# Performance work log

Measured on AMD Instinct MI355X. Metric: run time of the kernel, lower is better.

Reference implementation:

```python
import jax, jax.numpy as jnp
import numpy as np

N_VERT, D = 100000, 128
N_EDGE, K, R = 20000, 8, 4


def setup_inputs() -> dict:
    key = jax.random.key(0)
    ks = jax.random.split(key, 16)
    s = 0.05
    return {
        'feats': jax.random.normal(ks[0], (N_VERT, D), dtype=jnp.float32),
        'edge_members': jax.random.randint(ks[1], (N_EDGE, K), 0, N_VERT),
        'adj_members': jax.random.randint(ks[2], (N_EDGE, R, K), 0, N_VERT),
        'ids': jnp.arange(N_EDGE),
        'epoch': 10,
        # VertexConv params (Linear(d,1) each)
        'wq': jax.random.normal(ks[3], (D, 1)) * s, 'bq': jnp.zeros((1,)),
        'wk': jax.random.normal(ks[4], (D, 1)) * s, 'bk': jnp.zeros((1,)),
        'wv': jax.random.normal(ks[5], (D, 1)) * s, 'bv': jnp.zeros((1,)),
        # EdgeConv MLP: Linear(d, d//4) -> ReLU -> Linear(d//4, 1)
        'W1': jax.random.normal(ks[6], (D, D // 4)) * s, 'b1': jnp.zeros((D // 4,)),
        'W2': jax.random.normal(ks[7], (D // 4, 1)) * s, 'b2': jnp.zeros((1,)),
        # final classifier Linear(d, 2)
        'Wfc': jax.random.normal(ks[8], (D, 2)) * s, 'bfc': jnp.zeros((2,)),
    }


def _vertex_conv(feats, members, wq, bq, wk, bk, wv, bv):
    # members: [E, K] vertex indices; aggregates each hyperedge's vertices into one feature.
    f = feats[members]                         # [E,K,d] irregular gather
    q = f @ wq + bq                            # [E,K,1]
    k = f @ wk + bk                            # [E,K,1]
    v = f @ wv + bv                            # [E,K,1]
    # score[e,j,l] = q[e,j]*k[e,l]; original softmaxes over the K-1 "other" vertices (l != j)
    S = q * jnp.swapaxes(k, -1, -2)            # [E,K,K]
    S = jnp.where(jnp.eye(members.shape[-1], dtype=bool), -jnp.inf, S)
    a = jax.nn.softmax(S, axis=-1)             # [E,K,K]
    di = jnp.tanh(jnp.einsum('ejl,elo->ejo', a, v))  # [E,K,1] per-vertex scalar gate
    return (di * f).sum(axis=1)                # [E,d]


def reference(feats, edge_members, adj_members, ids, epoch,
              wq, bq, wk, bk, wv, bv, W1, b1, W2, b2, Wfc, bfc):
    n = edge_members.shape[0]
    # epoch >= wu_e(=0): hyperedge feature from edge_dict
    xn = _vertex_conv(feats, edge_members, wq, bq, wk, bk, wv, bv)   # [N,d]
    # epoch >= wu_a(=5): hyperedge features from each vertex's adjacent edges
    xe = _vertex_conv(feats, adj_members.reshape(n * R, K),
                      wq, bq, wk, bk, wv, bv).reshape(n, R, -1)       # [N,R,d]
    ft = jnp.concatenate([xn[:, None, :], xe], axis=1)                # [N,1+R,d]
    # EdgeConv: attention over the 1+R candidate hyperedge feats
    sc = jax.nn.relu(ft @ W1 + b1) @ W2 + b2                          # [N,1+R,1]
    a = jax.nn.softmax(sc, axis=1)
    h = (a * ft).sum(axis=1)                                          # [N,d]
    # dropout in eval mode (identity), then sigmoid(Linear(d,2))
    return jax.nn.sigmoid(h @ Wfc + bfc)                              # [N,2]
```

## Files before the change

kernel.cpp:

```cpp
#include <hip/hip_runtime.h>
#include <math.h>

#define KK 8
#define DD 128
#define RR 4
#define NG 5
#define HID 32
#define NSLOT 48

typedef __attribute__((ext_vector_type(8))) short short8_t;
typedef __attribute__((ext_vector_type(4))) float f32x4_t;

__device__ __forceinline__ unsigned short f2bf(float x) {
    unsigned int u = __float_as_uint(x);
    unsigned int r = (u + 0x7FFFu + ((u >> 16) & 1u)) >> 16;
    return (unsigned short)r;
}
__device__ __forceinline__ float bf2f(unsigned short u) {
    return __uint_as_float((unsigned int)u << 16);
}

__global__ __launch_bounds__(256) void proj_mfma(
    const float* __restrict__ feats, int n_vert, int n_tg,
    const float* __restrict__ wq, const float* __restrict__ wk,
    const float* __restrict__ wv, const float* __restrict__ Wfc,
    const float* __restrict__ W1,
    const float* __restrict__ bq, const float* __restrict__ bk,
    const float* __restrict__ bv,
    unsigned short* __restrict__ proj)
{
    __shared__ short Bsh[12 * 64 * 8];

    const int t = threadIdx.x;
    const int wave = t >> 6, lane = t & 63;
    const int row = lane & 15;
    const int kg  = lane >> 4;

    #pragma unroll
    for (int q = 0; q < 3; ++q) {
        const int p = t + q * 256;
        const int ntks = p >> 6, plane = p & 63;
        const int nt = ntks >> 2, ks = ntks & 3;
        const int n  = nt * 16 + (plane & 15);
        const int k0 = ks * 32 + (plane >> 4) * 8;
        short8_t v;
        #pragma unroll
        for (int j = 0; j < 8; ++j) {
            const int k = k0 + j;
            float val;
            if      (n == 0) val = wq[k];
            else if (n == 1) val = wk[k];
            else if (n == 2) val = wv[k];
            else if (n == 3) val = Wfc[2 * k];
            else if (n == 4) val = Wfc[2 * k + 1];
            else if (n < 37) val = W1[k * HID + (n - 5)];
            else             val = 0.f;
            v[j] = (short)f2bf(val);
        }
        *(short8_t*)&Bsh[p * 8] = v;
    }

    const float bq0 = bq[0], bk0 = bk[0], bv0 = bv[0];
    __syncthreads();

    for (int tg = blockIdx.x; tg < n_tg; tg += gridDim.x) {
        const int mbase = (tg * 4 + wave) * 16;
        if (mbase >= n_vert) continue;

        long long arow = (long long)(mbase + row);
        if (arow >= n_vert) arow = n_vert - 1;
        const float* ar = &feats[arow * DD + kg * 8];
        float4 araw[8];
        #pragma unroll
        for (int ks = 0; ks < 4; ++ks) {
            araw[2 * ks]     = *(const float4*)&ar[ks * 32];
            araw[2 * ks + 1] = *(const float4*)&ar[ks * 32 + 4];
        }

        short8_t afrag[4];
        #pragma unroll
        for (int ks = 0; ks < 4; ++ks) {
            const float4 x0 = araw[2 * ks], x1 = araw[2 * ks + 1];
            short8_t a;
            a[0] = (short)f2bf(x0.x); a[1] = (short)f2bf(x0.y);
            a[2] = (short)f2bf(x0.z); a[3] = (short)f2bf(x0.w);
            a[4] = (short)f2bf(x1.x); a[5] = (short)f2bf(x1.y);
            a[6] = (short)f2bf(x1.z); a[7] = (short)f2bf(x1.w);
            afrag[ks] = a;
        }

        #pragma unroll
        for (int nt = 0; nt < 3; ++nt) {
            f32x4_t acc = {0.f, 0.f, 0.f, 0.f};
            #pragma unroll
            for (int ks = 0; ks < 4; ++ks) {
                const short8_t b = *(const short8_t*)&Bsh[((nt * 4 + ks) * 64 + lane) * 8];
                acc = __builtin_amdgcn_mfma_f32_16x16x32_bf16(afrag[ks], b, acc, 0, 0, 0);
            }
            const int col = nt * 16 + row;
            if (col < 37) {
                const int slot = (col < 5) ? col : (col + 3);
                float badd = 0.f;
                if      (col == 0) badd = bq0;
                else if (col == 1) badd = bk0;
                else if (col == 2) badd = bv0;
                #pragma unroll
                for (int r = 0; r < 4; ++r) {
                    const int vr = mbase + kg * 4 + r;
                    if (vr < n_vert)
                        proj[(long long)vr * NSLOT + slot] = f2bf(acc[r] + badd);
                }
            }
        }
    }
}

__global__ __launch_bounds__(256) void edge_fused(
    const int* __restrict__ edge_members,
    const int* __restrict__ adj_members,
    const unsigned short* __restrict__ proj,
    const float* __restrict__ b1, const float* __restrict__ W2,
    const float* __restrict__ b2, const float* __restrict__ bfc,
    float* __restrict__ out, int n_edge)
{
    __shared__ int   vidS[4][NG * KK];
    __shared__ float diS [4][NG * KK];
    __shared__ float ftfcS[4][NG][2];
    __shared__ float scS [4][NG];

    const int t = threadIdx.x;
    const int w = t >> 6;
    const int lane = t & 63;
    const int e = blockIdx.x * 4 + w;
    if (e >= n_edge) return;

    const int g = lane >> 3;
    const int j = lane & 7;
    const bool act = lane < NG * KK;

    int vid = 0;
    if (act) vid = (g == 0) ? edge_members[e * KK + j]
                            : adj_members[((e * RR) + (g - 1)) * KK + j];

    const uint4 qpu = *(const uint4*)&proj[(long long)vid * NSLOT];

    if (act) vidS[w][lane] = vid;
    asm volatile("s_waitcnt lgkmcnt(0)" ::: "memory");

    const int m = lane & 31;
    const int h = lane >> 5;
    float pv2[3][KK];
    #pragma unroll
    for (int p = 0; p < 3; ++p) {
        const int grp = (p << 1) | h;
        if (grp < NG) {
            #pragma unroll
            for (int r = 0; r < KK; ++r) {
                const int vr = vidS[w][grp * KK + r];
                pv2[p][r] = bf2f(proj[(long long)vr * NSLOT + 8 + m]);
            }
        }
    }

    const float qv  = bf2f((unsigned short)(qpu.x & 0xFFFFu));
    const float kv  = bf2f((unsigned short)(qpu.x >> 16));
    const float vv  = bf2f((unsigned short)(qpu.y & 0xFFFFu));
    const float pf0 = bf2f((unsigned short)(qpu.y >> 16));
    const float pf1 = bf2f((unsigned short)(qpu.z & 0xFFFFu));

    float k8[KK], v8[KK];
    #pragma unroll
    for (int r = 0; r < KK; ++r) {
        k8[r] = __shfl(kv, (g << 3) + r);
        v8[r] = __shfl(vv, (g << 3) + r);
    }
    float mx = -1e30f;
    float s[KK];
    #pragma unroll
    for (int r = 0; r < KK; ++r) {
        s[r] = qv * k8[r];
        if (r != j) mx = fmaxf(mx, s[r]);
    }
    float den = 0.f, num = 0.f;
    #pragma unroll
    for (int r = 0; r < KK; ++r) {
        if (r == j) continue;
        const float ex = expf(s[r] - mx);
        den += ex;
        num += ex * v8[r];
    }
    const float di = tanhf(num / den);

    float px = di * pf0, py = di * pf1;
    #pragma unroll
    for (int mm = 4; mm >= 1; mm >>= 1) {
        px += __shfl_xor(px, mm);
        py += __shfl_xor(py, mm);
    }
    if (act) {
        diS[w][lane] = di;
        if (j == 0) { ftfcS[w][g][0] = px; ftfcS[w][g][1] = py; }
    }
    asm volatile("s_waitcnt lgkmcnt(0)" ::: "memory");

    const float b1m = b1[m];
    const float w2m = W2[m];
    #pragma unroll
    for (int p = 0; p < 3; ++p) {
        const int grp = (p << 1) | h;
        if (grp < NG) {
            float acc = 0.f;
            #pragma unroll
            for (int r = 0; r < KK; ++r)
                acc += diS[w][grp * KK + r] * pv2[p][r];
            float hid = fmaxf(acc + b1m, 0.f) * w2m;
            #pragma unroll
            for (int mm = 16; mm >= 1; mm >>= 1) hid += __shfl_xor(hid, mm);
            if (m == 0) scS[w][grp] = hid + b2[0];
        }
    }
    asm volatile("s_waitcnt lgkmcnt(0)" ::: "memory");

    if (lane < 2) {
        float sc0[NG];
        float m5 = -1e30f;
        #pragma unroll
        for (int gg = 0; gg < NG; ++gg) { sc0[gg] = scS[w][gg]; m5 = fmaxf(m5, sc0[gg]); }
        float ssum = 0.f;
        #pragma unroll
        for (int gg = 0; gg < NG; ++gg) { sc0[gg] = expf(sc0[gg] - m5); ssum += sc0[gg]; }
        const float inv = 1.f / ssum;
        float hc = 0.f;
        #pragma unroll
        for (int gg = 0; gg < NG; ++gg) hc += sc0[gg] * inv * ftfcS[w][gg][lane];
        const float z = hc + bfc[lane];
        out[e * 2 + lane] = 1.f / (1.f + expf(-z));
    }
}

extern "C" void kernel_launch(void* const* d_in, const int* in_sizes, int n_in,
                              void* d_out, int out_size, void* d_ws, size_t ws_size,
                              hipStream_t stream) {
    const float* feats        = (const float*)d_in[0];
    const int*   edge_members = (const int*)  d_in[1];
    const int*   adj_members  = (const int*)  d_in[2];
    const float* wq  = (const float*)d_in[5];
    const float* bq  = (const float*)d_in[6];
    const float* wk  = (const float*)d_in[7];
    const float* bk  = (const float*)d_in[8];
    const float* wv  = (const float*)d_in[9];
    const float* bv  = (const float*)d_in[10];
    const float* W1  = (const float*)d_in[11];
    const float* b1  = (const float*)d_in[12];
    const float* W2  = (const float*)d_in[13];
    const float* b2  = (const float*)d_in[14];
    const float* Wfc = (const float*)d_in[15];
    const float* bfc = (const float*)d_in[16];
    float* out = (float*)d_out;

    const int n_vert = in_sizes[0] / DD;
    const int n_edge = in_sizes[1] / KK;

    unsigned short* proj = (unsigned short*)d_ws;

    const int n_mtiles = (n_vert + 15) / 16;
    const int n_tg = (n_mtiles + 3) / 4;
    const int grid = (n_tg < 640) ? n_tg : 640;

    proj_mfma<<<grid, 256, 0, stream>>>(
        feats, n_vert, n_tg, wq, wk, wv, Wfc, W1, bq, bk, bv, proj);

    edge_fused<<<(n_edge + 3) / 4, 256, 0, stream>>>(
        edge_members, adj_members, proj, b1, W2, b2, bfc, out, n_edge);
}
```

Measured before the change: 41.85 us.

## Fuse projection and edge kernels into one cooperative kernel with grid sync

Merges the per-vertex projection phase and the per-edge attention phase into a single cooperative launch separated by a grid-wide barrier. Blocks then loop persistently over edge groups instead of launching one block per four edges. The aim is to remove the second kernel launch and the gap between the two kernels. In exchange it adds host-side occupancy queries and a grid sync, and the edge phase is limited to at most 640 persistent blocks. A fallback to the original two-kernel path remains if the cooperative launch fails.

```diff
diff --git a/kernel.cpp b/kernel.cpp
--- a/kernel.cpp
+++ b/kernel.cpp
@@ -1,4 +1,5 @@
 #include <hip/hip_runtime.h>
+#include <hip/hip_cooperative_groups.h>
 #include <math.h>
 
 #define KK 8
@@ -20,19 +21,16 @@
     return __uint_as_float((unsigned int)u << 16);
 }
 
-__global__ __launch_bounds__(256) void proj_mfma(
+__device__ __forceinline__ void proj_phase(
     const float* __restrict__ feats, int n_vert, int n_tg,
     const float* __restrict__ wq, const float* __restrict__ wk,
     const float* __restrict__ wv, const float* __restrict__ Wfc,
     const float* __restrict__ W1,
     const float* __restrict__ bq, const float* __restrict__ bk,
     const float* __restrict__ bv,
-    unsigned short* __restrict__ proj)
-{
-    __shared__ short Bsh[12 * 64 * 8];
-
-    const int t = threadIdx.x;
-    const int wave = t >> 6, lane = t & 63;
+    unsigned short* __restrict__ proj,
+    short* Bsh, int t, int wave, int lane, int bid, int gsz)
+{
     const int row = lane & 15;
     const int kg  = lane >> 4;
 
@@ -63,7 +61,7 @@
     const float bq0 = bq[0], bk0 = bk[0], bv0 = bv[0];
     __syncthreads();
 
-    for (int tg = blockIdx.x; tg < n_tg; tg += gridDim.x) {
+    for (int tg = bid; tg < n_tg; tg += gsz) {
         const int mbase = (tg * 4 + wave) * 16;
         if (mbase >= n_vert) continue;
 
@@ -115,28 +113,20 @@
     }
 }
 
-__global__ __launch_bounds__(256) void edge_fused(
-    const int* __restrict__ edge_members,
-    const int* __restrict__ adj_members,
+__device__ __forceinline__ void edge_body(
+    const int* __restrict__ edge_members, const int* __restrict__ adj_members,
     const unsigned short* __restrict__ proj,
     const float* __restrict__ b1, const float* __restrict__ W2,
     const float* __restrict__ b2, const float* __restrict__ bfc,
-    float* __restrict__ out, int n_edge)
-{
-    __shared__ int   vidS[4][NG * KK];
-    __shared__ float diS [4][NG * KK];
-    __shared__ float ftfcS[4][NG][2];
-    __shared__ float scS [4][NG];
-
-    const int t = threadIdx.x;
-    const int w = t >> 6;
-    const int lane = t & 63;
-    const int e = blockIdx.x * 4 + w;
-    if (e >= n_edge) return;
-
+    float* __restrict__ out, int n_edge, int e,
+    int w, int lane, int (*vidS)[NG * KK], float (*diS)[NG * KK],
+    float (*ftfcS)[NG][2], float (*scS)[NG])
+{
     const int g = lane >> 3;
     const int j = lane & 7;
     const bool act = lane < NG * KK;
+    const int m = lane & 31;
+    const int h = lane >> 5;
 
     int vid = 0;
     if (act) vid = (g == 0) ? edge_members[e * KK + j]
@@ -147,8 +137,6 @@
     if (act) vidS[w][lane] = vid;
     asm volatile("s_waitcnt lgkmcnt(0)" ::: "memory");
 
-    const int m = lane & 31;
-    const int h = lane >> 5;
     float pv2[3][KK];
     #pragma unroll
     for (int p = 0; p < 3; ++p) {
@@ -236,6 +224,77 @@
         const float z = hc + bfc[lane];
         out[e * 2 + lane] = 1.f / (1.f + expf(-z));
     }
+}
+
+__global__ __launch_bounds__(256) void dhg_all(
+    const float* __restrict__ feats, int n_vert, int n_tg,
+    const int* __restrict__ edge_members, const int* __restrict__ adj_members,
+    int n_edge, int n_eg,
+    const float* __restrict__ wq, const float* __restrict__ wk,
+    const float* __restrict__ wv, const float* __restrict__ Wfc,
+    const float* __restrict__ W1,
+    const float* __restrict__ bq, const float* __restrict__ bk,
+    const float* __restrict__ bv,
+    const float* __restrict__ b1, const float* __restrict__ W2,
+    const float* __restrict__ b2, const float* __restrict__ bfc,
+    unsigned short* __restrict__ proj, float* __restrict__ out)
+{
+    __shared__ short Bsh[12 * 64 * 8];
+    __shared__ int   vidS[4][NG * KK];
+    __shared__ float diS [4][NG * KK];
+    __shared__ float ftfcS[4][NG][2];
+    __shared__ float scS [4][NG];
+
+    const int t = threadIdx.x;
+    const int wave = t >> 6, lane = t & 63;
+
+    proj_phase(feats, n_vert, n_tg, wq, wk, wv, Wfc, W1, bq, bk, bv, proj,
+               Bsh, t, wave, lane, blockIdx.x, gridDim.x);
+
+    cooperative_groups::this_grid().sync();
+
+    for (int eg = blockIdx.x; eg < n_eg; eg += gridDim.x) {
+        const int e = eg * 4 + wave;
+        if (e >= n_edge) continue;
+        edge_body(edge_members, adj_members, proj, b1, W2, b2, bfc, out, n_edge,
+                  e, wave, lane, vidS, diS, ftfcS, scS);
+    }
+}
+
+__global__ __launch_bounds__(256) void proj_mfma(
+    const float* __restrict__ feats, int n_vert, int n_tg,
+    const float* __restrict__ wq, const float* __restrict__ wk,
+    const float* __restrict__ wv, const float* __restrict__ Wfc,
+    const float* __restrict__ W1,
+    const float* __restrict__ bq, const float* __restrict__ bk,
+    const float* __restrict__ bv,
+    unsigned short* __restrict__ proj)
+{
+    __shared__ short Bsh[12 * 64 * 8];
+    const int t = threadIdx.x;
+    proj_phase(feats, n_vert, n_tg, wq, wk, wv, Wfc, W1, bq, bk, bv, proj,
+               Bsh, t, t >> 6, t & 63, blockIdx.x, gridDim.x);
+}
+
+__global__ __launch_bounds__(256) void edge_fused(
+    const int* __restrict__ edge_members,
+    const int* __restrict__ adj_members,
+    const unsigned short* __restrict__ proj,
+    const float* __restrict__ b1, const float* __restrict__ W2,
+    const float* __restrict__ b2, const float* __restrict__ bfc,
+    float* __restrict__ out, int n_edge)
+{
+    __shared__ int   vidS[4][NG * KK];
+    __shared__ float diS [4][NG * KK];
+    __shared__ float ftfcS[4][NG][2];
+    __shared__ float scS [4][NG];
+
+    const int t = threadIdx.x;
+    const int w = t >> 6, lane = t & 63;
+    const int e = blockIdx.x * 4 + w;
+    if (e >= n_edge) return;
+    edge_body(edge_members, adj_members, proj, b1, W2, b2, bfc, out, n_edge,
+              e, w, lane, vidS, diS, ftfcS, scS);
 }
 
 extern "C" void kernel_launch(void* const* d_in, const int* in_sizes, int n_in,
@@ -258,18 +317,42 @@
     const float* bfc = (const float*)d_in[16];
     float* out = (float*)d_out;
 
-    const int n_vert = in_sizes[0] / DD;
-    const int n_edge = in_sizes[1] / KK;
+    int n_vert = in_sizes[0] / DD;
+    int n_edge = in_sizes[1] / KK;
 
     unsigned short* proj = (unsigned short*)d_ws;
 
-    const int n_mtiles = (n_vert + 15) / 16;
-    const int n_tg = (n_mtiles + 3) / 4;
-    const int grid = (n_tg < 640) ? n_tg : 640;
-
-    proj_mfma<<<grid, 256, 0, stream>>>(
-        feats, n_vert, n_tg, wq, wk, wv, Wfc, W1, bq, bk, bv, proj);
-
-    edge_fused<<<(n_edge + 3) / 4, 256, 0, stream>>>(
-        edge_members, adj_members, proj, b1, W2, b2, bfc, out, n_edge);
-}
+    int n_mtiles = (n_vert + 15) / 16;
+    int n_tg = (n_mtiles + 3) / 4;
+    int n_eg = (n_edge + 3) / 4;
+
+    bool coop_ok = false;
+    int maxBlk = 0, nCU = 0;
+    if (hipOccupancyMaxActiveBlocksPerMultiprocessor(&maxBlk, (const void*)dhg_all, 256, 0)
+            == hipSuccess && maxBlk > 0 &&
+        hipDeviceGetAttribute(&nCU, hipDeviceAttributeMultiprocessorCount, 0)
+            == hipSuccess && nCU > 0) {
+        int grid = maxBlk * nCU;
+        if (grid > 640) grid = 640;
+        if (grid > n_tg) grid = n_tg;
+        void* args[] = {
+            (void*)&feats, (void*)&n_vert, (void*)&n_tg,
+            (void*)&edge_members, (void*)&adj_members, (void*)&n_edge, (void*)&n_eg,
+            (void*)&wq, (void*)&wk, (void*)&wv, (void*)&Wfc, (void*)&W1,
+            (void*)&bq, (void*)&bk, (void*)&bv,
+            (void*)&b1, (void*)&W2, (void*)&b2, (void*)&bfc,
+            (void*)&proj, (void*)&out
+        };
+        if (hipLaunchCooperativeKernel((const void*)dhg_all, dim3(grid), dim3(256),
+                                       args, 0, stream) == hipSuccess)
+            coop_ok = true;
+    }
+
+    if (!coop_ok) {
+        const int grid = (n_tg < 640) ? n_tg : 640;
+        proj_mfma<<<grid, 256, 0, stream>>>(
+            feats, n_vert, n_tg, wq, wk, wv, Wfc, W1, bq, bk, bv, proj);
+        edge_fused<<<(n_edge + 3) / 4, 256, 0, stream>>>(
+            edge_members, adj_members, proj, b1, W2, b2, bfc, out, n_edge);
+    }
+}
```

New measurement: 136.7 us. 3.27x slower.

## Replace LDS staging in edge kernel with wave shuffles and vectorized proj loads

Applied to the files above, without the earlier changes.

The edge kernel drops all shared-memory staging (vertex ids, gates, partial scores) and redistributes data across lanes with shuffles instead. Each lane now loads four contiguous bf16 hidden-projection values per member vertex (8-byte loads) rather than one scalar per lane, and the W1 reduction becomes cross-lane xor shuffles. The final softmax and classifier run in registers on every lane, so the LDS round-trips and waitcnt barriers go away. The cost is more shuffle instructions and a different load pattern.

```diff
diff --git a/kernel.cpp b/kernel.cpp
--- a/kernel.cpp
+++ b/kernel.cpp
@@ -123,11 +123,6 @@
     const float* __restrict__ b2, const float* __restrict__ bfc,
     float* __restrict__ out, int n_edge)
 {
-    __shared__ int   vidS[4][NG * KK];
-    __shared__ float diS [4][NG * KK];
-    __shared__ float ftfcS[4][NG][2];
-    __shared__ float scS [4][NG];
-
     const int t = threadIdx.x;
     const int w = t >> 6;
     const int lane = t & 63;
@@ -144,22 +139,11 @@
 
     const uint4 qpu = *(const uint4*)&proj[(long long)vid * NSLOT];
 
-    if (act) vidS[w][lane] = vid;
-    asm volatile("s_waitcnt lgkmcnt(0)" ::: "memory");
-
-    const int m = lane & 31;
-    const int h = lane >> 5;
-    float pv2[3][KK];
-    #pragma unroll
-    for (int p = 0; p < 3; ++p) {
-        const int grp = (p << 1) | h;
-        if (grp < NG) {
-            #pragma unroll
-            for (int r = 0; r < KK; ++r) {
-                const int vr = vidS[w][grp * KK + r];
-                pv2[p][r] = bf2f(proj[(long long)vr * NSLOT + 8 + m]);
-            }
-        }
+    uint2 p1raw[NG];
+    #pragma unroll
+    for (int grp = 0; grp < NG; ++grp) {
+        const int vr = __shfl(vid, grp * KK + g);
+        p1raw[grp] = *(const uint2*)&proj[(long long)vr * NSLOT + 8 + j * 4];
     }
 
     const float qv  = bf2f((unsigned short)(qpu.x & 0xFFFFu));
@@ -197,43 +181,57 @@
         px += __shfl_xor(px, mm);
         py += __shfl_xor(py, mm);
     }
-    if (act) {
-        diS[w][lane] = di;
-        if (j == 0) { ftfcS[w][g][0] = px; ftfcS[w][g][1] = py; }
-    }
-    asm volatile("s_waitcnt lgkmcnt(0)" ::: "memory");
-
-    const float b1m = b1[m];
-    const float w2m = W2[m];
-    #pragma unroll
-    for (int p = 0; p < 3; ++p) {
-        const int grp = (p << 1) | h;
-        if (grp < NG) {
-            float acc = 0.f;
-            #pragma unroll
-            for (int r = 0; r < KK; ++r)
-                acc += diS[w][grp * KK + r] * pv2[p][r];
-            float hid = fmaxf(acc + b1m, 0.f) * w2m;
-            #pragma unroll
-            for (int mm = 16; mm >= 1; mm >>= 1) hid += __shfl_xor(hid, mm);
-            if (m == 0) scS[w][grp] = hid + b2[0];
-        }
-    }
-    asm volatile("s_waitcnt lgkmcnt(0)" ::: "memory");
-
+
+    const float4 b1v = *(const float4*)&b1[j * 4];
+    const float4 w2v = *(const float4*)&W2[j * 4];
+    const float b20 = b2[0];
+    float sc5[NG];
+    #pragma unroll
+    for (int grp = 0; grp < NG; ++grp) {
+        const float dr = __shfl(di, grp * KK + g);
+        const uint2 u = p1raw[grp];
+        float p0 = dr * bf2f((unsigned short)(u.x & 0xFFFFu));
+        float p1_ = dr * bf2f((unsigned short)(u.x >> 16));
+        float p2 = dr * bf2f((unsigned short)(u.y & 0xFFFFu));
+        float p3 = dr * bf2f((unsigned short)(u.y >> 16));
+        #pragma unroll
+        for (int mk = 8; mk <= 32; mk <<= 1) {
+            p0  += __shfl_xor(p0,  mk);
+            p1_ += __shfl_xor(p1_, mk);
+            p2  += __shfl_xor(p2,  mk);
+            p3  += __shfl_xor(p3,  mk);
+        }
+        float hid = fmaxf(p0  + b1v.x, 0.f) * w2v.x
+                  + fmaxf(p1_ + b1v.y, 0.f) * w2v.y
+                  + fmaxf(p2  + b1v.z, 0.f) * w2v.z
+                  + fmaxf(p3  + b1v.w, 0.f) * w2v.w;
+        #pragma unroll
+        for (int mk = 1; mk <= 4; mk <<= 1)
+            hid += __shfl_xor(hid, mk);
+        sc5[grp] = hid + b20;
+    }
+
+    float fx5[NG], fy5[NG];
+    #pragma unroll
+    for (int gg = 0; gg < NG; ++gg) {
+        fx5[gg] = __shfl(px, gg * 8);
+        fy5[gg] = __shfl(py, gg * 8);
+    }
+
+    float m5 = sc5[0];
+    #pragma unroll
+    for (int gg = 1; gg < NG; ++gg) m5 = fmaxf(m5, sc5[gg]);
+    float ssum = 0.f, h0 = 0.f, h1 = 0.f;
+    #pragma unroll
+    for (int gg = 0; gg < NG; ++gg) {
+        const float a = expf(sc5[gg] - m5);
+        ssum += a;
+        h0 += a * fx5[gg];
+        h1 += a * fy5[gg];
+    }
+    const float inv = 1.f / ssum;
     if (lane < 2) {
-        float sc0[NG];
-        float m5 = -1e30f;
-        #pragma unroll
-        for (int gg = 0; gg < NG; ++gg) { sc0[gg] = scS[w][gg]; m5 = fmaxf(m5, sc0[gg]); }
-        float ssum = 0.f;
-        #pragma unroll
-        for (int gg = 0; gg < NG; ++gg) { sc0[gg] = expf(sc0[gg] - m5); ssum += sc0[gg]; }
-        const float inv = 1.f / ssum;
-        float hc = 0.f;
-        #pragma unroll
-        for (int gg = 0; gg < NG; ++gg) hc += sc0[gg] * inv * ftfcS[w][gg][lane];
-        const float z = hc + bfc[lane];
+        const float z = ((lane == 0) ? h0 : h1) * inv + bfc[lane];
         out[e * 2 + lane] = 1.f / (1.f + expf(-z));
     }
 }
```

New measurement: 49.34 us. 17.9% more time.
